# Performance work log

Hardware: AMD Instinct MI355X
Metric: run time of the kernel (lower is better)

Reference implementation:

```python
import jax, jax.numpy as jnp
import numpy as np

N = 100000      # nodes
D = 128         # num_hidden_channels == num_output_feats
H = 4           # attention heads
HD = D // H     # head dim = 32
KNN = 20        # in-edges per node
E = N * KNN
BN_EPS = 1e-5


def setup_inputs() -> dict:
    key = jax.random.key(0)
    ks = jax.random.split(key, 20)
    s = 1.0 / np.sqrt(D)
    f = jax.random.normal(ks[0], (N, D), jnp.float32)
    src = jax.random.randint(ks[1], (E,), 0, N, dtype=jnp.int32)
    dst = jnp.repeat(jnp.arange(N, dtype=jnp.int32), KNN)  # knn in-edges per node
    return {
        "f": f,
        "src": src,
        "dst": dst,
        "bn1_gamma": jax.random.normal(ks[2], (D,), jnp.float32) * 0.1 + 1.0,
        "bn1_beta": jax.random.normal(ks[3], (D,), jnp.float32) * 0.1,
        "bn1_mean": jax.random.normal(ks[4], (D,), jnp.float32) * 0.1,
        "bn1_var": jax.random.uniform(ks[5], (D,), jnp.float32, 0.5, 1.5),
        "Wq": jax.random.normal(ks[6], (D, D), jnp.float32) * s,
        "Wk": jax.random.normal(ks[7], (D, D), jnp.float32) * s,
        "Wv": jax.random.normal(ks[8], (D, D), jnp.float32) * s,
        "Wo": jax.random.normal(ks[9], (D, D), jnp.float32) * s,
        "bo": jax.random.normal(ks[10], (D,), jnp.float32) * 0.01,
        "bn2_gamma": jax.random.normal(ks[11], (D,), jnp.float32) * 0.1 + 1.0,
        "bn2_beta": jax.random.normal(ks[12], (D,), jnp.float32) * 0.1,
        "bn2_mean": jax.random.normal(ks[13], (D,), jnp.float32) * 0.1,
        "bn2_var": jax.random.uniform(ks[14], (D,), jnp.float32, 0.5, 1.5),
        "W1": jax.random.normal(ks[15], (D, 2 * D), jnp.float32) * s,
        "W2": jax.random.normal(ks[16], (2 * D, D), jnp.float32) * (1.0 / np.sqrt(2 * D)),
    }


def _bn(x, gamma, beta, mean, var):
    # eval-mode BatchNorm1d with running statistics
    return (x - mean) * (gamma / jnp.sqrt(var + BN_EPS)) + beta


def reference(f, src, dst, bn1_gamma, bn1_beta, bn1_mean, bn1_var,
              Wq, Wk, Wv, Wo, bo,
              bn2_gamma, bn2_beta, bn2_mean, bn2_var, W1, W2):
    n = f.shape[0]
    h = _bn(f, bn1_gamma, bn1_beta, bn1_mean, bn1_var)
    q = (h @ Wq).reshape(n, H, HD)
    k = (h @ Wk).reshape(n, H, HD)
    v = (h @ Wv).reshape(n, H, HD)
    # edge-wise score: K[src] . Q[dst]  -> [E, H]
    score = jnp.einsum('ehd,ehd->eh', k[src], q[dst]) / np.sqrt(HD)
    score = jnp.exp(jnp.clip(score, -5.0, 5.0))
    # scatter-sum weighted V and normalizer to destination nodes
    wV = jax.ops.segment_sum(v[src] * score[:, :, None], dst, num_segments=n)  # [N,H,HD]
    z = jax.ops.segment_sum(score, dst, num_segments=n)                        # [N,H]
    attn = (wV / (z[:, :, None] + 1e-6)).reshape(n, D)
    node = attn @ Wo + bo
    node = f + node  # residual 1 (dropout is identity in eval)
    h2 = _bn(node, bn2_gamma, bn2_beta, bn2_mean, bn2_var)
    mlp = jax.nn.silu(h2 @ W1) @ W2
    return node + mlp  # residual 2
```

## Files before the change

### kernel.cpp

```cpp
#include <hip/hip_runtime.h>
#include <hip/hip_bf16.h>

#define NN 100000
#define DD 128
#define KNN 20

typedef unsigned short u16;
typedef __attribute__((ext_vector_type(8))) __bf16 bf16x8;
typedef __attribute__((ext_vector_type(4))) float f32x4;
typedef __attribute__((ext_vector_type(4))) unsigned short u16x4;
typedef __attribute__((ext_vector_type(8))) unsigned short u16x8;

__device__ __forceinline__ float b2f(u16 b) {
  unsigned int u = ((unsigned int)b) << 16;
  float f;
  __builtin_memcpy(&f, &u, 4);
  return f;
}
__device__ __forceinline__ u16 f2b(float f) {
  unsigned int u;
  __builtin_memcpy(&u, &f, 4);
  u += 0x7fffu + ((u >> 16) & 1u);
  return (u16)(u >> 16);
}

__device__ __forceinline__ void stage_frag(const float* __restrict__ W, int wstride,
                                           int colbase, u16* __restrict__ dst, int f) {
  int lane = f & 63;
  int t2 = f >> 6;
  int ksl = t2 & 3;
  int ct = (t2 >> 2) & 7;
  int kc = t2 >> 5;
  int ks = kc * 4 + ksl;
  int quad = lane >> 4, l16 = lane & 15;
  const float* src = W + (size_t)(ks * 32 + quad * 8) * wstride + colbase + ct * 16 + l16;
  u16x8 o;
#pragma unroll
  for (int j = 0; j < 8; j++) o[j] = f2b(src[(size_t)j * wstride]);
  *(u16x8*)(dst + (size_t)f * 8) = o;
}

__global__ __launch_bounds__(256) void stage_weights_kernel(
    const float* __restrict__ Wq, const float* __restrict__ Wk, const float* __restrict__ Wv,
    const float* __restrict__ Wo, const float* __restrict__ W1, const float* __restrict__ W2,
    const float* __restrict__ g1, const float* __restrict__ b1,
    const float* __restrict__ m1, const float* __restrict__ v1,
    const float* __restrict__ g2, const float* __restrict__ b2,
    const float* __restrict__ m2, const float* __restrict__ v2,
    const float* __restrict__ bo,
    u16* __restrict__ WTf,
    float* __restrict__ sc1, float* __restrict__ bb1,
    float* __restrict__ sc2, float* __restrict__ bb2, float* __restrict__ bof)
{
  int t = blockIdx.x * 256 + threadIdx.x;
  if (t < 2048)       stage_frag(Wq, 128, 0,   WTf + 0,     t);
  else if (t < 4096)  stage_frag(Wk, 128, 0,   WTf + 16384, t - 2048);
  else if (t < 6144)  stage_frag(Wv, 128, 0,   WTf + 32768, t - 4096);
  else if (t < 8192)  stage_frag(Wo, 128, 0,   WTf + 49152, t - 6144);
  else if (t < 10240) stage_frag(W1, 256, 0,   WTf + 65536, t - 8192);
  else if (t < 12288) stage_frag(W1, 256, 128, WTf + 81920, t - 10240);
  else if (t < 16384) stage_frag(W2, 128, 0,   WTf + 98304, t - 12288);
  else if (t < 16512) {
    int c = t - 16384;
    float s1 = g1[c] * rsqrtf(v1[c] + 1e-5f);
    sc1[c] = s1; bb1[c] = b1[c] - m1[c] * s1;
    float s2 = g2[c] * rsqrtf(v2[c] + 1e-5f);
    sc2[c] = s2; bb2[c] = b2[c] - m2[c] * s2;
    bof[c] = bo[c];
  }
}

__global__ __launch_bounds__(256) void qkv_kernel(
    const float* __restrict__ f, const u16* __restrict__ WTf,
    const float* __restrict__ sc1, const float* __restrict__ bb1,
    u16* __restrict__ qb, u16* __restrict__ kvb)
{
  const int tid = threadIdx.x;
  const int wave = tid >> 6, lane = tid & 63, quad = lane >> 4, l16 = lane & 15;
  const int rowbase = blockIdx.x * 128 + wave * 32;

  bf16x8 af[2][4];
#pragma unroll
  for (int ks = 0; ks < 4; ks++) {
    int ch = ks * 32 + quad * 8;
    f32x4 s0 = *(const f32x4*)(sc1 + ch), s1 = *(const f32x4*)(sc1 + ch + 4);
    f32x4 c0 = *(const f32x4*)(bb1 + ch), c1 = *(const f32x4*)(bb1 + ch + 4);
#pragma unroll
    for (int rt = 0; rt < 2; rt++) {
      int arow = rowbase + rt * 16 + l16;
      if (arow >= NN) arow = NN - 1;
      const float* fp = f + (size_t)arow * DD + ch;
      f32x4 x0 = *(const f32x4*)(fp), x1 = *(const f32x4*)(fp + 4);
      u16x8 hv;
#pragma unroll
      for (int j = 0; j < 4; j++) {
        hv[j]     = f2b(x0[j] * s0[j] + c0[j]);
        hv[j + 4] = f2b(x1[j] * s1[j] + c1[j]);
      }
      af[rt][ks] = __builtin_bit_cast(bf16x8, hv);
    }
  }

  u16x4 ks16[2][8];
#pragma unroll
  for (int m = 0; m < 3; m++) {
    f32x4 acc[2][8];
#pragma unroll
    for (int rt = 0; rt < 2; rt++)
#pragma unroll
      for (int ct = 0; ct < 8; ct++) acc[rt][ct] = (f32x4){0.f, 0.f, 0.f, 0.f};
#pragma unroll
    for (int ct = 0; ct < 8; ct++)
#pragma unroll
      for (int ks = 0; ks < 4; ks++) {
        bf16x8 wf = *(const bf16x8*)(WTf + (size_t)m * 16384 + ((ct * 4 + ks) * 64 + lane) * 8);
        acc[0][ct] = __builtin_amdgcn_mfma_f32_16x16x32_bf16(wf, af[0][ks], acc[0][ct], 0, 0, 0);
        acc[1][ct] = __builtin_amdgcn_mfma_f32_16x16x32_bf16(wf, af[1][ks], acc[1][ct], 0, 0, 0);
      }
#pragma unroll
    for (int rt = 0; rt < 2; rt++)
#pragma unroll
      for (int ct = 0; ct < 8; ct++) {
        int row = rowbase + rt * 16 + l16;
        int ch0 = ct * 16 + quad * 4;
        if (m == 0) {
          if (row < NN) {
            u16x4 o;
#pragma unroll
            for (int r = 0; r < 4; r++) o[r] = f2b(acc[rt][ct][r]);
            *(u16x4*)(qb + (size_t)row * DD + ch0) = o;
          }
        } else if (m == 1) {
          u16x4 o;
#pragma unroll
          for (int r = 0; r < 4; r++) o[r] = f2b(acc[rt][ct][r]);
          ks16[rt][ct] = o;
        } else {
          if (row < NN) {
            u16x8 o;
#pragma unroll
            for (int r = 0; r < 4; r++) {
              o[2 * r] = ks16[rt][ct][r];
              o[2 * r + 1] = f2b(acc[rt][ct][r]);
            }
            *(u16x8*)(kvb + (size_t)row * 256 + ch0 * 2) = o;
          }
        }
      }
  }
}

__global__ __launch_bounds__(256) void attn_kernel(
    const u16* __restrict__ q, const u16* __restrict__ kv,
    const int* __restrict__ src, u16* __restrict__ attnb)
{
  const int node = blockIdx.x * 8 + (threadIdx.x >> 5);
  const int sub = threadIdx.x & 31;
  const int c0 = sub * 4;
  const size_t qbase = (size_t)node * DD + c0;

  u16x4 qr = *(const u16x4*)(q + qbase);
  const float qv0 = b2f(qr[0]), qv1 = b2f(qr[1]), qv2 = b2f(qr[2]), qv3 = b2f(qr[3]);

  int sv[KNN];
  const int* sp = src + (size_t)node * KNN;
#pragma unroll
  for (int j = 0; j < KNN; j++) sv[j] = sp[j];

  float a0 = 0.f, a1 = 0.f, a2 = 0.f, a3 = 0.f, z = 0.f;
  const float inv_sqrt_hd = 0.17677669529663687f;
#pragma unroll 10
  for (int j = 0; j < KNN; j++) {
    u16x8 kvr = *(const u16x8*)(kv + (size_t)sv[j] * 256 + c0 * 2);
    float p = b2f(kvr[0]) * qv0 + b2f(kvr[2]) * qv1 + b2f(kvr[4]) * qv2 + b2f(kvr[6]) * qv3;
    p += __shfl_xor(p, 1);
    p += __shfl_xor(p, 2);
    p += __shfl_xor(p, 4);
    float sc = __expf(fminf(fmaxf(p * inv_sqrt_hd, -5.f), 5.f));
    z += sc;
    a0 += sc * b2f(kvr[1]);
    a1 += sc * b2f(kvr[3]);
    a2 += sc * b2f(kvr[5]);
    a3 += sc * b2f(kvr[7]);
  }
  float inv = 1.f / (z + 1e-6f);
  u16x4 o;
  o[0] = f2b(a0 * inv); o[1] = f2b(a1 * inv);
  o[2] = f2b(a2 * inv); o[3] = f2b(a3 * inv);
  *(u16x4*)(attnb + qbase) = o;
}

__global__ __launch_bounds__(256) void mlp_kernel(
    const u16* __restrict__ attnb, const float* __restrict__ f, const u16* __restrict__ WTf,
    const float* __restrict__ bof, const float* __restrict__ sc2, const float* __restrict__ bb2,
    float* __restrict__ out)
{
  __shared__ u16 T[8704];
  const int tid = threadIdx.x;
  const int wave = tid >> 6, lane = tid & 63, quad = lane >> 4, l16 = lane & 15;
  const int rowbase = blockIdx.x * 128 + wave * 32;
  u16* tile = T + wave * 2176;

  bf16x8 af[2][4];
#pragma unroll
  for (int rt = 0; rt < 2; rt++) {
    int arow = rowbase + rt * 16 + l16;
    if (arow >= NN) arow = NN - 1;
    const u16* ap = attnb + (size_t)arow * DD + quad * 8;
#pragma unroll
    for (int ks = 0; ks < 4; ks++) af[rt][ks] = *(const bf16x8*)(ap + ks * 32);
  }

  f32x4 nv[2][8];
#pragma unroll
  for (int rt = 0; rt < 2; rt++)
#pragma unroll
    for (int ct = 0; ct < 8; ct++) nv[rt][ct] = (f32x4){0.f, 0.f, 0.f, 0.f};
#pragma unroll
  for (int ct = 0; ct < 8; ct++)
#pragma unroll
    for (int ks = 0; ks < 4; ks++) {
      bf16x8 wf = *(const bf16x8*)(WTf + 49152 + ((ct * 4 + ks) * 64 + lane) * 8);
      nv[0][ct] = __builtin_amdgcn_mfma_f32_16x16x32_bf16(wf, af[0][ks], nv[0][ct], 0, 0, 0);
      nv[1][ct] = __builtin_amdgcn_mfma_f32_16x16x32_bf16(wf, af[1][ks], nv[1][ct], 0, 0, 0);
    }

  u16x4 h4s[8];
#pragma unroll
  for (int ct = 0; ct < 8; ct++) {
    int ch0 = ct * 16 + quad * 4;
    f32x4 bo4 = *(const f32x4*)(bof + ch0);
    f32x4 s4  = *(const f32x4*)(sc2 + ch0);
    f32x4 b4  = *(const f32x4*)(bb2 + ch0);
#pragma unroll
    for (int rt = 0; rt < 2; rt++) {
      int row = rowbase + rt * 16 + l16;
      int rl = row < NN ? row : NN - 1;
      f32x4 f4 = *(const f32x4*)(f + (size_t)rl * DD + ch0);
      nv[rt][ct] += bo4 + f4;
      u16x4 h4;
#pragma unroll
      for (int r = 0; r < 4; r++) h4[r] = f2b(nv[rt][ct][r] * s4[r] + b4[r]);
      if (rt == 0) *(u16x4*)(tile + l16 * 136 + ch0) = h4;
      else h4s[ct] = h4;
    }
  }
  bf16x8 hf[2][4];
#pragma unroll
  for (int ks = 0; ks < 4; ks++) hf[0][ks] = *(const bf16x8*)(tile + l16 * 136 + ks * 32 + quad * 8);
#pragma unroll
  for (int ct = 0; ct < 8; ct++) *(u16x4*)(tile + l16 * 136 + ct * 16 + quad * 4) = h4s[ct];
#pragma unroll
  for (int ks = 0; ks < 4; ks++) hf[1][ks] = *(const bf16x8*)(tile + l16 * 136 + ks * 32 + quad * 8);

  f32x4 acc3[2][8];
#pragma unroll
  for (int rt = 0; rt < 2; rt++)
#pragma unroll
    for (int ct = 0; ct < 8; ct++) acc3[rt][ct] = (f32x4){0.f, 0.f, 0.f, 0.f};

#pragma unroll
  for (int m = 0; m < 2; m++) {
    f32x4 acc2[2][8];
#pragma unroll
    for (int rt = 0; rt < 2; rt++)
#pragma unroll
      for (int ct = 0; ct < 8; ct++) acc2[rt][ct] = (f32x4){0.f, 0.f, 0.f, 0.f};
#pragma unroll
    for (int ct = 0; ct < 8; ct++)
#pragma unroll
      for (int ks = 0; ks < 4; ks++) {
        bf16x8 wf = *(const bf16x8*)(WTf + 65536 + m * 16384 + ((ct * 4 + ks) * 64 + lane) * 8);
        acc2[0][ct] = __builtin_amdgcn_mfma_f32_16x16x32_bf16(wf, hf[0][ks], acc2[0][ct], 0, 0, 0);
        acc2[1][ct] = __builtin_amdgcn_mfma_f32_16x16x32_bf16(wf, hf[1][ks], acc2[1][ct], 0, 0, 0);
      }
    u16x4 i4s[8];
#pragma unroll
    for (int ct = 0; ct < 8; ct++) {
      int ch0 = ct * 16 + quad * 4;
      u16x4 i0, i1;
#pragma unroll
      for (int r = 0; r < 4; r++) {
        float x0 = acc2[0][ct][r], x1 = acc2[1][ct][r];
        i0[r] = f2b(x0 / (1.f + __expf(-x0)));
        i1[r] = f2b(x1 / (1.f + __expf(-x1)));
      }
      *(u16x4*)(tile + l16 * 136 + ch0) = i0;
      i4s[ct] = i1;
    }
    bf16x8 iff[2][4];
#pragma unroll
    for (int ksl = 0; ksl < 4; ksl++) iff[0][ksl] = *(const bf16x8*)(tile + l16 * 136 + ksl * 32 + quad * 8);
#pragma unroll
    for (int ct = 0; ct < 8; ct++) *(u16x4*)(tile + l16 * 136 + ct * 16 + quad * 4) = i4s[ct];
#pragma unroll
    for (int ksl = 0; ksl < 4; ksl++) iff[1][ksl] = *(const bf16x8*)(tile + l16 * 136 + ksl * 32 + quad * 8);
#pragma unroll
    for (int ct = 0; ct < 8; ct++)
#pragma unroll
      for (int ksl = 0; ksl < 4; ksl++) {
        bf16x8 wf = *(const bf16x8*)(WTf + 98304 + ((m * 32 + ct * 4 + ksl) * 64 + lane) * 8);
        acc3[0][ct] = __builtin_amdgcn_mfma_f32_16x16x32_bf16(wf, iff[0][ksl], acc3[0][ct], 0, 0, 0);
        acc3[1][ct] = __builtin_amdgcn_mfma_f32_16x16x32_bf16(wf, iff[1][ksl], acc3[1][ct], 0, 0, 0);
      }
  }

#pragma unroll
  for (int rt = 0; rt < 2; rt++)
#pragma unroll
    for (int ct = 0; ct < 8; ct++) {
      int row = rowbase + rt * 16 + l16;
      if (row < NN) {
        int ch0 = ct * 16 + quad * 4;
        *(f32x4*)(out + (size_t)row * DD + ch0) = acc3[rt][ct] + nv[rt][ct];
      }
    }
}

extern "C" void kernel_launch(void* const* d_in, const int* in_sizes, int n_in,
                              void* d_out, int out_size, void* d_ws, size_t ws_size,
                              hipStream_t stream) {
  const float* f  = (const float*)d_in[0];
  const int* src  = (const int*)d_in[1];
  const float* g1 = (const float*)d_in[3];
  const float* b1 = (const float*)d_in[4];
  const float* m1 = (const float*)d_in[5];
  const float* v1 = (const float*)d_in[6];
  const float* Wq = (const float*)d_in[7];
  const float* Wk = (const float*)d_in[8];
  const float* Wv = (const float*)d_in[9];
  const float* Wo = (const float*)d_in[10];
  const float* bo = (const float*)d_in[11];
  const float* g2 = (const float*)d_in[12];
  const float* b2 = (const float*)d_in[13];
  const float* m2 = (const float*)d_in[14];
  const float* v2 = (const float*)d_in[15];
  const float* W1 = (const float*)d_in[16];
  const float* W2 = (const float*)d_in[17];
  float* out = (float*)d_out;

  char* ws = (char*)d_ws;
  u16*  WTf = (u16*)(ws + 0);
  float* sc1 = (float*)(ws + 262144);
  float* bb1 = (float*)(ws + 262656);
  float* sc2 = (float*)(ws + 263168);
  float* bb2 = (float*)(ws + 263680);
  float* bof = (float*)(ws + 264192);
  u16*  qb    = (u16*)(ws + 1048576);
  u16*  kvb   = (u16*)(ws + 26648576);
  u16*  attnb = (u16*)(ws + 77848576);

  const int ggrid = (NN + 127) / 128;

  stage_weights_kernel<<<65, 256, 0, stream>>>(
      Wq, Wk, Wv, Wo, W1, W2, g1, b1, m1, v1, g2, b2, m2, v2, bo,
      WTf, sc1, bb1, sc2, bb2, bof);

  qkv_kernel<<<ggrid, 256, 0, stream>>>(f, WTf, sc1, bb1, qb, kvb);

  attn_kernel<<<NN / 8, 256, 0, stream>>>(qb, kvb, src, attnb);

  mlp_kernel<<<ggrid, 256, 0, stream>>>(attnb, f, WTf, bof, sc2, bb2, out);
}
```

Baseline: 525.5 us.

## Halve rows per wave and split MLP kernel into Wo and FFN kernels

Each wave now handles 16 rows instead of 32, which halves the accumulator register footprint in the QKV and MLP kernels and should raise occupancy. The fused mlp_kernel is split into wo_kernel, which writes the fp32 node residual and the bf16 BN2 output, and mlp2_kernel, which runs the FFN and adds the residual back. These intermediates reuse the q/kv workspace buffers. The split adds an extra global write and read of node (fp32) and h2 per row, plus one more launch, and each weight fragment load is now amortized over fewer rows.

```diff
diff --git a/kernel.cpp b/kernel.cpp
--- a/kernel.cpp
+++ b/kernel.cpp
@@ -77,76 +77,68 @@
 {
   const int tid = threadIdx.x;
   const int wave = tid >> 6, lane = tid & 63, quad = lane >> 4, l16 = lane & 15;
-  const int rowbase = blockIdx.x * 128 + wave * 32;
-
-  bf16x8 af[2][4];
+  const int rowbase = blockIdx.x * 64 + wave * 16;
+  int arow = rowbase + l16;
+  if (arow >= NN) arow = NN - 1;
+
+  bf16x8 af[4];
 #pragma unroll
   for (int ks = 0; ks < 4; ks++) {
     int ch = ks * 32 + quad * 8;
     f32x4 s0 = *(const f32x4*)(sc1 + ch), s1 = *(const f32x4*)(sc1 + ch + 4);
     f32x4 c0 = *(const f32x4*)(bb1 + ch), c1 = *(const f32x4*)(bb1 + ch + 4);
-#pragma unroll
-    for (int rt = 0; rt < 2; rt++) {
-      int arow = rowbase + rt * 16 + l16;
-      if (arow >= NN) arow = NN - 1;
-      const float* fp = f + (size_t)arow * DD + ch;
-      f32x4 x0 = *(const f32x4*)(fp), x1 = *(const f32x4*)(fp + 4);
-      u16x8 hv;
-#pragma unroll
-      for (int j = 0; j < 4; j++) {
-        hv[j]     = f2b(x0[j] * s0[j] + c0[j]);
-        hv[j + 4] = f2b(x1[j] * s1[j] + c1[j]);
-      }
-      af[rt][ks] = __builtin_bit_cast(bf16x8, hv);
-    }
-  }
-
-  u16x4 ks16[2][8];
+    const float* fp = f + (size_t)arow * DD + ch;
+    f32x4 x0 = *(const f32x4*)(fp), x1 = *(const f32x4*)(fp + 4);
+    u16x8 hv;
+#pragma unroll
+    for (int j = 0; j < 4; j++) {
+      hv[j]     = f2b(x0[j] * s0[j] + c0[j]);
+      hv[j + 4] = f2b(x1[j] * s1[j] + c1[j]);
+    }
+    af[ks] = __builtin_bit_cast(bf16x8, hv);
+  }
+
+  const int srow = rowbase + l16;
+  u16x4 ks16[8];
 #pragma unroll
   for (int m = 0; m < 3; m++) {
-    f32x4 acc[2][8];
-#pragma unroll
-    for (int rt = 0; rt < 2; rt++)
-#pragma unroll
-      for (int ct = 0; ct < 8; ct++) acc[rt][ct] = (f32x4){0.f, 0.f, 0.f, 0.f};
+    f32x4 acc[8];
+#pragma unroll
+    for (int ct = 0; ct < 8; ct++) acc[ct] = (f32x4){0.f, 0.f, 0.f, 0.f};
 #pragma unroll
     for (int ct = 0; ct < 8; ct++)
 #pragma unroll
       for (int ks = 0; ks < 4; ks++) {
         bf16x8 wf = *(const bf16x8*)(WTf + (size_t)m * 16384 + ((ct * 4 + ks) * 64 + lane) * 8);
-        acc[0][ct] = __builtin_amdgcn_mfma_f32_16x16x32_bf16(wf, af[0][ks], acc[0][ct], 0, 0, 0);
-        acc[1][ct] = __builtin_amdgcn_mfma_f32_16x16x32_bf16(wf, af[1][ks], acc[1][ct], 0, 0, 0);
-      }
-#pragma unroll
-    for (int rt = 0; rt < 2; rt++)
-#pragma unroll
-      for (int ct = 0; ct < 8; ct++) {
-        int row = rowbase + rt * 16 + l16;
-        int ch0 = ct * 16 + quad * 4;
-        if (m == 0) {
-          if (row < NN) {
-            u16x4 o;
-#pragma unroll
-            for (int r = 0; r < 4; r++) o[r] = f2b(acc[rt][ct][r]);
-            *(u16x4*)(qb + (size_t)row * DD + ch0) = o;
+        acc[ct] = __builtin_amdgcn_mfma_f32_16x16x32_bf16(wf, af[ks], acc[ct], 0, 0, 0);
+      }
+#pragma unroll
+    for (int ct = 0; ct < 8; ct++) {
+      int ch0 = ct * 16 + quad * 4;
+      if (m == 0) {
+        if (srow < NN) {
+          u16x4 o;
+#pragma unroll
+          for (int r = 0; r < 4; r++) o[r] = f2b(acc[ct][r]);
+          *(u16x4*)(qb + (size_t)srow * DD + ch0) = o;
+        }
+      } else if (m == 1) {
+        u16x4 o;
+#pragma unroll
+        for (int r = 0; r < 4; r++) o[r] = f2b(acc[ct][r]);
+        ks16[ct] = o;
+      } else {
+        if (srow < NN) {
+          u16x8 o;
+#pragma unroll
+          for (int r = 0; r < 4; r++) {
+            o[2 * r] = ks16[ct][r];
+            o[2 * r + 1] = f2b(acc[ct][r]);
           }
-        } else if (m == 1) {
-          u16x4 o;
-#pragma unroll
-          for (int r = 0; r < 4; r++) o[r] = f2b(acc[rt][ct][r]);
-          ks16[rt][ct] = o;
-        } else {
-          if (row < NN) {
-            u16x8 o;
-#pragma unroll
-            for (int r = 0; r < 4; r++) {
-              o[2 * r] = ks16[rt][ct][r];
-              o[2 * r + 1] = f2b(acc[rt][ct][r]);
-            }
-            *(u16x8*)(kvb + (size_t)row * 256 + ch0 * 2) = o;
-          }
+          *(u16x8*)(kvb + (size_t)srow * 256 + ch0 * 2) = o;
         }
       }
+    }
   }
 }
 
@@ -190,131 +182,118 @@
   *(u16x4*)(attnb + qbase) = o;
 }
 
-__global__ __launch_bounds__(256) void mlp_kernel(
+__global__ __launch_bounds__(256) void wo_kernel(
     const u16* __restrict__ attnb, const float* __restrict__ f, const u16* __restrict__ WTf,
     const float* __restrict__ bof, const float* __restrict__ sc2, const float* __restrict__ bb2,
-    float* __restrict__ out)
-{
-  __shared__ u16 T[8704];
+    float* __restrict__ node, u16* __restrict__ h2)
+{
   const int tid = threadIdx.x;
   const int wave = tid >> 6, lane = tid & 63, quad = lane >> 4, l16 = lane & 15;
-  const int rowbase = blockIdx.x * 128 + wave * 32;
-  u16* tile = T + wave * 2176;
-
-  bf16x8 af[2][4];
-#pragma unroll
-  for (int rt = 0; rt < 2; rt++) {
-    int arow = rowbase + rt * 16 + l16;
-    if (arow >= NN) arow = NN - 1;
-    const u16* ap = attnb + (size_t)arow * DD + quad * 8;
-#pragma unroll
-    for (int ks = 0; ks < 4; ks++) af[rt][ks] = *(const bf16x8*)(ap + ks * 32);
-  }
-
-  f32x4 nv[2][8];
-#pragma unroll
-  for (int rt = 0; rt < 2; rt++)
-#pragma unroll
-    for (int ct = 0; ct < 8; ct++) nv[rt][ct] = (f32x4){0.f, 0.f, 0.f, 0.f};
+  const int rowbase = blockIdx.x * 64 + wave * 16;
+  int arow = rowbase + l16;
+  if (arow >= NN) arow = NN - 1;
+
+  bf16x8 af[4];
+  const u16* ap = attnb + (size_t)arow * DD + quad * 8;
+#pragma unroll
+  for (int ks = 0; ks < 4; ks++) af[ks] = *(const bf16x8*)(ap + ks * 32);
+
+  f32x4 nv[8];
+#pragma unroll
+  for (int ct = 0; ct < 8; ct++) nv[ct] = (f32x4){0.f, 0.f, 0.f, 0.f};
 #pragma unroll
   for (int ct = 0; ct < 8; ct++)
 #pragma unroll
     for (int ks = 0; ks < 4; ks++) {
       bf16x8 wf = *(const bf16x8*)(WTf + 49152 + ((ct * 4 + ks) * 64 + lane) * 8);
-      nv[0][ct] = __builtin_amdgcn_mfma_f32_16x16x32_bf16(wf, af[0][ks], nv[0][ct], 0, 0, 0);
-      nv[1][ct] = __builtin_amdgcn_mfma_f32_16x16x32_bf16(wf, af[1][ks], nv[1][ct], 0, 0, 0);
-    }
-
-  u16x4 h4s[8];
+      nv[ct] = __builtin_amdgcn_mfma_f32_16x16x32_bf16(wf, af[ks], nv[ct], 0, 0, 0);
+    }
+
+  const int srow = rowbase + l16;
 #pragma unroll
   for (int ct = 0; ct < 8; ct++) {
     int ch0 = ct * 16 + quad * 4;
     f32x4 bo4 = *(const f32x4*)(bof + ch0);
     f32x4 s4  = *(const f32x4*)(sc2 + ch0);
     f32x4 b4  = *(const f32x4*)(bb2 + ch0);
-#pragma unroll
-    for (int rt = 0; rt < 2; rt++) {
-      int row = rowbase + rt * 16 + l16;
-      int rl = row < NN ? row : NN - 1;
-      f32x4 f4 = *(const f32x4*)(f + (size_t)rl * DD + ch0);
-      nv[rt][ct] += bo4 + f4;
+    f32x4 f4 = *(const f32x4*)(f + (size_t)arow * DD + ch0);
+    f32x4 n4 = nv[ct] + bo4 + f4;
+    if (srow < NN) {
+      *(f32x4*)(node + (size_t)srow * DD + ch0) = n4;
       u16x4 h4;
 #pragma unroll
-      for (int r = 0; r < 4; r++) h4[r] = f2b(nv[rt][ct][r] * s4[r] + b4[r]);
-      if (rt == 0) *(u16x4*)(tile + l16 * 136 + ch0) = h4;
-      else h4s[ct] = h4;
-    }
-  }
-  bf16x8 hf[2][4];
-#pragma unroll
-  for (int ks = 0; ks < 4; ks++) hf[0][ks] = *(const bf16x8*)(tile + l16 * 136 + ks * 32 + quad * 8);
-#pragma unroll
-  for (int ct = 0; ct < 8; ct++) *(u16x4*)(tile + l16 * 136 + ct * 16 + quad * 4) = h4s[ct];
-#pragma unroll
-  for (int ks = 0; ks < 4; ks++) hf[1][ks] = *(const bf16x8*)(tile + l16 * 136 + ks * 32 + quad * 8);
-
-  f32x4 acc3[2][8];
-#pragma unroll
-  for (int rt = 0; rt < 2; rt++)
-#pragma unroll
-    for (int ct = 0; ct < 8; ct++) acc3[rt][ct] = (f32x4){0.f, 0.f, 0.f, 0.f};
+      for (int r = 0; r < 4; r++) h4[r] = f2b(n4[r] * s4[r] + b4[r]);
+      *(u16x4*)(h2 + (size_t)srow * DD + ch0) = h4;
+    }
+  }
+}
+
+__global__ __launch_bounds__(256) void mlp2_kernel(
+    const u16* __restrict__ h2, const float* __restrict__ node, const u16* __restrict__ WTf,
+    float* __restrict__ out)
+{
+  __shared__ u16 T[8704];
+  const int tid = threadIdx.x;
+  const int wave = tid >> 6, lane = tid & 63, quad = lane >> 4, l16 = lane & 15;
+  const int rowbase = blockIdx.x * 64 + wave * 16;
+  u16* tile = T + wave * 2176;
+  int arow = rowbase + l16;
+  if (arow >= NN) arow = NN - 1;
+
+  bf16x8 hf[4];
+  const u16* hp = h2 + (size_t)arow * DD + quad * 8;
+#pragma unroll
+  for (int ks = 0; ks < 4; ks++) hf[ks] = *(const bf16x8*)(hp + ks * 32);
+
+  f32x4 acc3[8];
+#pragma unroll
+  for (int ct = 0; ct < 8; ct++) acc3[ct] = (f32x4){0.f, 0.f, 0.f, 0.f};
 
 #pragma unroll
   for (int m = 0; m < 2; m++) {
-    f32x4 acc2[2][8];
-#pragma unroll
-    for (int rt = 0; rt < 2; rt++)
-#pragma unroll
-      for (int ct = 0; ct < 8; ct++) acc2[rt][ct] = (f32x4){0.f, 0.f, 0.f, 0.f};
+    f32x4 acc2[8];
+#pragma unroll
+    for (int ct = 0; ct < 8; ct++) acc2[ct] = (f32x4){0.f, 0.f, 0.f, 0.f};
 #pragma unroll
     for (int ct = 0; ct < 8; ct++)
 #pragma unroll
       for (int ks = 0; ks < 4; ks++) {
         bf16x8 wf = *(const bf16x8*)(WTf + 65536 + m * 16384 + ((ct * 4 + ks) * 64 + lane) * 8);
-        acc2[0][ct] = __builtin_amdgcn_mfma_f32_16x16x32_bf16(wf, hf[0][ks], acc2[0][ct], 0, 0, 0);
-        acc2[1][ct] = __builtin_amdgcn_mfma_f32_16x16x32_bf16(wf, hf[1][ks], acc2[1][ct], 0, 0, 0);
-      }
-    u16x4 i4s[8];
+        acc2[ct] = __builtin_amdgcn_mfma_f32_16x16x32_bf16(wf, hf[ks], acc2[ct], 0, 0, 0);
+      }
 #pragma unroll
     for (int ct = 0; ct < 8; ct++) {
       int ch0 = ct * 16 + quad * 4;
-      u16x4 i0, i1;
+      u16x4 i4;
 #pragma unroll
       for (int r = 0; r < 4; r++) {
-        float x0 = acc2[0][ct][r], x1 = acc2[1][ct][r];
-        i0[r] = f2b(x0 / (1.f + __expf(-x0)));
-        i1[r] = f2b(x1 / (1.f + __expf(-x1)));
-      }
-      *(u16x4*)(tile + l16 * 136 + ch0) = i0;
-      i4s[ct] = i1;
-    }
-    bf16x8 iff[2][4];
-#pragma unroll
-    for (int ksl = 0; ksl < 4; ksl++) iff[0][ksl] = *(const bf16x8*)(tile + l16 * 136 + ksl * 32 + quad * 8);
-#pragma unroll
-    for (int ct = 0; ct < 8; ct++) *(u16x4*)(tile + l16 * 136 + ct * 16 + quad * 4) = i4s[ct];
-#pragma unroll
-    for (int ksl = 0; ksl < 4; ksl++) iff[1][ksl] = *(const bf16x8*)(tile + l16 * 136 + ksl * 32 + quad * 8);
+        float x = acc2[ct][r];
+        i4[r] = f2b(x / (1.f + __expf(-x)));
+      }
+      *(u16x4*)(tile + l16 * 136 + ch0) = i4;
+    }
+    bf16x8 iff[4];
+#pragma unroll
+    for (int ksl = 0; ksl < 4; ksl++)
+      iff[ksl] = *(const bf16x8*)(tile + l16 * 136 + ksl * 32 + quad * 8);
 #pragma unroll
     for (int ct = 0; ct < 8; ct++)
 #pragma unroll
       for (int ksl = 0; ksl < 4; ksl++) {
         bf16x8 wf = *(const bf16x8*)(WTf + 98304 + ((m * 32 + ct * 4 + ksl) * 64 + lane) * 8);
-        acc3[0][ct] = __builtin_amdgcn_mfma_f32_16x16x32_bf16(wf, iff[0][ksl], acc3[0][ct], 0, 0, 0);
-        acc3[1][ct] = __builtin_amdgcn_mfma_f32_16x16x32_bf16(wf, iff[1][ksl], acc3[1][ct], 0, 0, 0);
-      }
-  }
-
-#pragma unroll
-  for (int rt = 0; rt < 2; rt++)
+        acc3[ct] = __builtin_amdgcn_mfma_f32_16x16x32_bf16(wf, iff[ksl], acc3[ct], 0, 0, 0);
+      }
+  }
+
+  const int srow = rowbase + l16;
+  if (srow < NN) {
 #pragma unroll
     for (int ct = 0; ct < 8; ct++) {
-      int row = rowbase + rt * 16 + l16;
-      if (row < NN) {
-        int ch0 = ct * 16 + quad * 4;
-        *(f32x4*)(out + (size_t)row * DD + ch0) = acc3[rt][ct] + nv[rt][ct];
-      }
-    }
+      int ch0 = ct * 16 + quad * 4;
+      f32x4 n4 = *(const f32x4*)(node + (size_t)srow * DD + ch0);
+      *(f32x4*)(out + (size_t)srow * DD + ch0) = acc3[ct] + n4;
+    }
+  }
 }
 
 extern "C" void kernel_launch(void* const* d_in, const int* in_sizes, int n_in,
@@ -346,19 +325,19 @@
   float* sc2 = (float*)(ws + 263168);
   float* bb2 = (float*)(ws + 263680);
   float* bof = (float*)(ws + 264192);
-  u16*  qb    = (u16*)(ws + 1048576);
-  u16*  kvb   = (u16*)(ws + 26648576);
-  u16*  attnb = (u16*)(ws + 77848576);
-
-  const int ggrid = (NN + 127) / 128;
+  u16*   qb    = (u16*)(ws + (1u << 20));
+  u16*   kvb   = (u16*)(ws + 27262976u);
+  u16*   attnb = (u16*)(ws + 80740352u);
+  u16*   h2    = qb;
+  float* node  = (float*)kvb;
 
   stage_weights_kernel<<<65, 256, 0, stream>>>(
       Wq, Wk, Wv, Wo, W1, W2, g1, b1, m1, v1, g2, b2, m2, v2, bo,
       WTf, sc1, bb1, sc2, bb2, bof);
 
+  const int ggrid = (NN + 63) / 64;
   qkv_kernel<<<ggrid, 256, 0, stream>>>(f, WTf, sc1, bb1, qb, kvb);
-
   attn_kernel<<<NN / 8, 256, 0, stream>>>(qb, kvb, src, attnb);
-
-  mlp_kernel<<<ggrid, 256, 0, stream>>>(attnb, f, WTf, bof, sc2, bb2, out);
-}
+  wo_kernel<<<ggrid, 256, 0, stream>>>(attnb, f, WTf, bof, sc2, bb2, node, h2);
+  mlp2_kernel<<<ggrid, 256, 0, stream>>>(h2, node, WTf, out);
+}
```

Result: faster. 463.5 us (-11.8%).
